# Optimization experiments

Hardware: AMD Instinct MI355X
Metric: run time of the kernel (lower is better)

## Reference

```python
import jax, jax.numpy as jnp
import numpy as np

C = 100000
D = 512
KEEP_RATIO = 0.5
EPS = 1.1920929e-07  # torch.finfo(float32).eps
K = max(1, int(C * KEEP_RATIO))


def _l2norm(x):
    # F.normalize(dim=-1): x / max(||x||, eps)
    n = jnp.linalg.norm(x, axis=-1, keepdims=True)
    return x / jnp.maximum(n, EPS)


def setup_inputs() -> dict:
    key = jax.random.key(0)
    k1, k2, k3 = jax.random.split(key, 3)
    tensor = jax.random.normal(k1, (1024, D), dtype=jnp.float32)
    target = jax.random.randint(k2, (1024,), 0, C, dtype=jnp.int32)
    # xavier_normal_ on (C, D): std = sqrt(2 / (C + D))
    std = np.sqrt(2.0 / (C + D)).astype(np.float32)
    weight = jax.random.normal(k3, (C, D), dtype=jnp.float32) * std
    return {"tensor": tensor, "target": target, "weight": weight}


def reference(tensor, target, weight):
    # --- target mining (no-grad in original) ---
    t_n = _l2norm(tensor)            # (B, D)
    w_n = _l2norm(weight)            # (C, D)
    # max over batch of cosine similarity -> per-class score (C,)
    scores = jnp.max(jnp.einsum("bd,cd->bc", t_n, w_n), axis=0)
    # ground-truth classes always kept
    scores = scores.at[target].set(2.0)
    _, topk_idx = jax.lax.top_k(scores, K)
    subsample = jnp.sort(topk_idx)                       # (K,) ascending
    # remap targets into subsampled index space (targets guaranteed present)
    new_target = jnp.searchsorted(subsample, target).astype(jnp.int32)
    # --- head ---
    w_sub = weight[subsample]                            # (K, D) gather
    logits = jnp.einsum("bd,kd->bk", _l2norm(tensor), _l2norm(w_sub))
    return logits, new_target
```

## Files before the change

### kernel.cpp

```cpp
#include <hip/hip_runtime.h>

#define C_CLS 100000
#define D_DIM 512
#define B_ROWS 1024
#define K_KEEP 50000
#define EPS_F 1.1920929e-07f
#define MB_CT 64
#define BAND 2e-3f
#define DELTA 4e-4f
#define RMAX 32768

typedef short v8s __attribute__((ext_vector_type(8)));
typedef float v4f __attribute__((ext_vector_type(4)));

struct Ctrl { unsigned prefix; unsigned need; };

__device__ __forceinline__ unsigned key_of(float f){
  unsigned u = __float_as_uint(f);
  return (u & 0x80000000u) ? ~u : (u | 0x80000000u);
}
__device__ __forceinline__ float key_inv(unsigned k){
  unsigned u = (k & 0x80000000u) ? (k & 0x7FFFFFFFu) : ~k;
  return __uint_as_float(u);
}
__device__ __forceinline__ unsigned short f2bf_rne(float f){
  unsigned u = __float_as_uint(f);
  unsigned r = (u + 0x7FFFu + ((u >> 16) & 1u)) >> 16;
  return (unsigned short)r;
}
__device__ __forceinline__ float bf2f(unsigned short h){
  return __uint_as_float(((unsigned)h) << 16);
}


__global__ __launch_bounds__(64) void norm_t_kernel(const float* __restrict__ t, float* __restrict__ tn,
                                                    unsigned short* __restrict__ tnph, unsigned short* __restrict__ tnpl,
                                                    const int* __restrict__ tgt, unsigned* __restrict__ keys){
  int row = blockIdx.x, lane = threadIdx.x;
  if (lane == 0) atomicMax(&keys[tgt[row]], key_of(2.0f));
  const float4* p = (const float4*)(t + (size_t)row * D_DIM);
  float4 a = p[lane*2+0], b = p[lane*2+1];
  float s = a.x*a.x + a.y*a.y + a.z*a.z + a.w*a.w
          + b.x*b.x + b.y*b.y + b.z*b.z + b.w*b.w;
  #pragma unroll
  for (int off = 32; off; off >>= 1) s += __shfl_xor(s, off);
  float den = fmaxf(sqrtf(s), EPS_F);
  float o[8] = {a.x/den, a.y/den, a.z/den, a.w/den, b.x/den, b.y/den, b.z/den, b.w/den};
  float4* q = (float4*)(tn + (size_t)row * D_DIM);
  q[lane*2+0] = make_float4(o[0],o[1],o[2],o[3]);
  q[lane*2+1] = make_float4(o[4],o[5],o[6],o[7]);
  v8s hv, lv;
  #pragma unroll
  for (int j = 0; j < 8; ++j){
    unsigned short h = f2bf_rne(o[j]);
    hv[j] = (short)h;
    lv[j] = (short)f2bf_rne(o[j] - bf2f(h));
  }
  size_t di = (size_t)((row & ~15) + (lane >> 2)) * 512 + (lane & 3) * 128 + (row & 15) * 8;
  *(v8s*)(tnph + di) = hv;
  *(v8s*)(tnpl + di) = lv;
}

__device__ __forceinline__ void load_a4(const unsigned short* __restrict__ tp, int b0, int ks, int lane, v8s* dst){
  #pragma unroll
  for (int i = 0; i < 4; ++i){
    int t = b0 + i*16 + (ks >> 5);
    dst[i] = *(const v8s*)(tp + (size_t)t * 512 + lane * 8);
  }
}

__global__ __launch_bounds__(256, 2) void mine_kernel(
    const unsigned short* __restrict__ tnph, const unsigned short* __restrict__ tnpl,
    const float* __restrict__ w, unsigned* __restrict__ keys,
    float* __restrict__ S, float* __restrict__ winv_g){
  __shared__ unsigned short lw[MB_CT * D_DIM];
  __shared__ float wn[MB_CT];
  const int tid = threadIdx.x;
  const int lane = tid & 63;
  const int cb = blockIdx.x * MB_CT;
  #pragma unroll
  for (int st = 0; st < 16; ++st){
    int g = tid + st * 256;
    int row = g >> 6, fc = g & 63;
    int c = cb + row; if (c >= C_CLS) c = C_CLS - 1;
    const float4* src = (const float4*)(w + (size_t)c * D_DIM + fc * 8);
    float4 v0 = src[0], v1 = src[1];
    float vv[8] = {v0.x,v0.y,v0.z,v0.w,v1.x,v1.y,v1.z,v1.w};
    float s = 0.f;
    #pragma unroll
    for (int j = 0; j < 8; ++j) s += vv[j]*vv[j];
    #pragma unroll
    for (int off = 32; off; off >>= 1) s += __shfl_xor(s, off);
    if (lane == 0) wn[row] = 1.0f / fmaxf(sqrtf(s), EPS_F);
    v8s hv;
    #pragma unroll
    for (int j = 0; j < 8; ++j) hv[j] = (short)f2bf_rne(vv[j]);
    int csw = fc ^ (row & 7);
    *(v8s*)&lw[(size_t)row * D_DIM + csw * 8] = hv;
  }
  __syncthreads();
  if (tid < MB_CT && cb + tid < C_CLS) winv_g[cb + tid] = wn[tid];

  const int wv = tid >> 6;
  const int lr = lane & 15, lg = lane >> 4;
  const int bbase = wv * 256;
  float runmax[4] = {-1e30f,-1e30f,-1e30f,-1e30f};
  v4f acc[4][4];
  #pragma unroll
  for (int j = 0; j < 4; ++j)
    #pragma unroll
    for (int i = 0; i < 4; ++i) acc[j][i] = (v4f){0.f,0.f,0.f,0.f};

  v8s cah[4], cal[4];
  load_a4(tnph, bbase, 0, lane, cah);
  load_a4(tnpl, bbase, 0, lane, cal);

  for (int it = 0; it < 64; ++it){
    const int chunk = it >> 4, ks = (it & 15) << 5;
    v8s nah[4], nal[4];
    if (it < 63){
      int nit = it + 1;
      int nb0 = bbase + (nit >> 4) * 64, nks = (nit & 15) << 5;
      load_a4(tnph, nb0, nks, lane, nah);
      load_a4(tnpl, nb0, nks, lane, nal);
    }
    v8s bh[4];
    #pragma unroll
    for (int j = 0; j < 4; ++j){
      int row = j*16 + lr;
      int ch = ((ks >> 3) + lg) ^ (lr & 7);
      bh[j] = *(const v8s*)&lw[(size_t)row * D_DIM + ch * 8];
    }
    #pragma unroll
    for (int j = 0; j < 4; ++j)
      #pragma unroll
      for (int i = 0; i < 4; ++i){
        acc[j][i] = __builtin_amdgcn_mfma_f32_16x16x32_bf16(cah[i], bh[j], acc[j][i], 0, 0, 0);
        acc[j][i] = __builtin_amdgcn_mfma_f32_16x16x32_bf16(cal[i], bh[j], acc[j][i], 0, 0, 0);
      }
    if ((it & 15) == 15){
      int b0 = bbase + chunk * 64;
      #pragma unroll
      for (int j = 0; j < 4; ++j){
        float m = acc[j][0][0];
        #pragma unroll
        for (int i = 0; i < 4; ++i)
          #pragma unroll
          for (int r = 0; r < 4; ++r) m = fmaxf(m, acc[j][i][r]);
        runmax[j] = fmaxf(runmax[j], m);
        int cls = cb + j*16 + lr;
        if (cls < C_CLS){
          #pragma unroll
          for (int i = 0; i < 4; ++i){
            float4 v = make_float4(acc[j][i][0], acc[j][i][1], acc[j][i][2], acc[j][i][3]);
            *(float4*)(S + (size_t)cls * B_ROWS + b0 + i*16 + lg*4) = v;
          }
        }
        #pragma unroll
        for (int i = 0; i < 4; ++i) acc[j][i] = (v4f){0.f,0.f,0.f,0.f};
      }
    }
    if (it < 63){
      #pragma unroll
      for (int i = 0; i < 4; ++i){ cah[i] = nah[i]; cal[i] = nal[i]; }
    }
  }
  #pragma unroll
  for (int j = 0; j < 4; ++j){
    float m = runmax[j];
    m = fmaxf(m, __shfl_xor(m, 16));
    m = fmaxf(m, __shfl_xor(m, 32));
    int cls = cb + j*16 + lr;
    if (lg == 0 && cls < C_CLS)
      atomicMax(&keys[cls], key_of(m * wn[j*16 + lr]));
  }
}

__global__ __launch_bounds__(256) void histsel_kernel(const unsigned* __restrict__ keys, unsigned* __restrict__ hist,
                                                      unsigned* __restrict__ done, Ctrl* __restrict__ ctrl, int shift){
  __shared__ unsigned h[256];
  __shared__ int lastf;
  int t = threadIdx.x;
  h[t] = 0u;
  __syncthreads();
  unsigned himask = (shift >= 24) ? 0u : (0xFFFFFFFFu << (shift + 8));
  unsigned prefix = (shift == 24) ? 0u : (ctrl->prefix & himask);
  for (int c = blockIdx.x * 256 + t; c < C_CLS; c += gridDim.x * 256){
    unsigned k = keys[c];
    if ((k & himask) == prefix) atomicAdd(&h[(k >> shift) & 255], 1u);
  }
  __syncthreads();
  if (h[t]) atomicAdd(&hist[t], h[t]);
  __threadfence();
  if (t == 0) lastf = (atomicAdd(done, 1u) == (unsigned)(gridDim.x - 1));
  __syncthreads();
  if (lastf){
    unsigned v = __hip_atomic_load(&hist[t], __ATOMIC_RELAXED, __HIP_MEMORY_SCOPE_AGENT);
    h[t] = v;
    __syncthreads();
    if (t == 0){
      unsigned need = (shift == 24) ? (unsigned)K_KEEP : ctrl->need;
      unsigned pfx  = (shift == 24) ? 0u : ctrl->prefix;
      unsigned cum = 0; int b;
      for (b = 255; b >= 0; --b){
        if (cum + h[b] >= need) break;
        cum += h[b];
      }
      if (b < 0) b = 0;
      ctrl->prefix = pfx | ((unsigned)b << shift);
      ctrl->need = need - cum;
      __hip_atomic_store(done, 0u, __ATOMIC_RELAXED, __HIP_MEMORY_SCOPE_AGENT);
    }
    __hip_atomic_store(&hist[t], 0u, __ATOMIC_RELAXED, __HIP_MEMORY_SCOPE_AGENT);
  }
}

__global__ void band_kernel(const unsigned* __restrict__ keys, const Ctrl* __restrict__ ctrl,
                            int* __restrict__ rlist, int* __restrict__ rcount){
  int c = blockIdx.x * 256 + threadIdx.x;
  if (c >= C_CLS) return;
  unsigned k = keys[c];
  if (k == key_of(2.0f)) return;
  float t = key_inv(ctrl->prefix);
  if (fabsf(key_inv(k) - t) <= BAND){
    int i = atomicAdd(rcount, 1);
    if (i < RMAX) rlist[i] = c;
  }
}

__global__ __launch_bounds__(256) void refine_kernel(
    const float* __restrict__ tn, const float* __restrict__ w,
    const float* __restrict__ winv, const float* __restrict__ S,
    const int* __restrict__ rlist, const int* __restrict__ rcount,
    unsigned* __restrict__ keys){
  __shared__ float red[256];
  __shared__ double dred[256];
  __shared__ int cand[32];
  __shared__ int ncand;
  int n = *rcount; if (n > RMAX) n = RMAX;
  int t = threadIdx.x;
  for (int i = blockIdx.x; i < n; i += gridDim.x){
    int c = rlist[i];
    const v4f* srow = (const v4f*)(S + (size_t)c * B_ROWS);
    v4f sv = srow[t];
    float m = fmaxf(fmaxf(sv[0],sv[1]), fmaxf(sv[2],sv[3]));
    red[t] = m; __syncthreads();
    for (int off2 = 128; off2; off2 >>= 1){
      if (t < off2) red[t] = fmaxf(red[t], red[t+off2]);
      __syncthreads();
    }
    float thr = red[0] - DELTA;
    if (t == 0) ncand = 0;
    __syncthreads();
    #pragma unroll
    for (int e = 0; e < 4; ++e){
      if (sv[e] >= thr){
        int ci = atomicAdd(&ncand, 1);
        if (ci < 32) cand[ci] = t*4 + e;
      }
    }
    __syncthreads();
    int nc = ncand; if (nc > 32) nc = 32;
    const float* wrow = w + (size_t)c * D_DIM;
    double w0 = (double)wrow[2*t], w1 = (double)wrow[2*t+1];
    double best = -1e300;
    for (int q = 0; q < nc; ++q){
      int b = cand[q];
      const float* tr = tn + (size_t)b * D_DIM;
      double p = fma((double)tr[2*t], w0, (double)tr[2*t+1] * w1);
      dred[t] = p; __syncthreads();
      for (int off2 = 128; off2; off2 >>= 1){
        if (t < off2) dred[t] += dred[t+off2];
        __syncthreads();
      }
      if (t == 0) best = fmax(best, dred[0]);
      __syncthreads();
    }
    if (t == 0) keys[c] = key_of((float)(best * (double)winv[c]));
    __syncthreads();
  }
}

__global__ __launch_bounds__(256) void scanA_kernel(const unsigned* __restrict__ keys, const Ctrl* __restrict__ ctrl,
                                                    uint2* __restrict__ bsum2, unsigned* __restrict__ done2, int nb){
  __shared__ unsigned red[256];
  __shared__ int lastf;
  int t = threadIdx.x;
  unsigned T = ctrl->prefix;
  int base = blockIdx.x * 1024 + t * 4;
  unsigned pack = 0;
  #pragma unroll
  for (int j = 0; j < 4; ++j){
    int c = base + j;
    if (c < C_CLS){
      unsigned k = keys[c];
      if (k > T) pack += 0x10000u;
      else if (k == T) pack += 1u;
    }
  }
  red[t] = pack; __syncthreads();
  for (int off = 128; off; off >>= 1){
    if (t < off) red[t] += red[t + off];
    __syncthreads();
  }
  if (t == 0) bsum2[blockIdx.x] = make_uint2(red[0] >> 16, red[0] & 0xFFFFu);
  __threadfence();
  if (t == 0) lastf = (atomicAdd(done2, 1u) == (unsigned)(gridDim.x - 1));
  __syncthreads();
  if (lastf && t == 0){
    unsigned rg = 0, re = 0;
    for (int i = 0; i < nb; ++i){
      unsigned vx = __hip_atomic_load(&bsum2[i].x, __ATOMIC_RELAXED, __HIP_MEMORY_SCOPE_AGENT);
      unsigned vy = __hip_atomic_load(&bsum2[i].y, __ATOMIC_RELAXED, __HIP_MEMORY_SCOPE_AGENT);
      __hip_atomic_store(&bsum2[i].x, rg, __ATOMIC_RELAXED, __HIP_MEMORY_SCOPE_AGENT);
      __hip_atomic_store(&bsum2[i].y, re, __ATOMIC_RELAXED, __HIP_MEMORY_SCOPE_AGENT);
      rg += vx; re += vy;
    }
    __hip_atomic_store(done2, 0u, __ATOMIC_RELAXED, __HIP_MEMORY_SCOPE_AGENT);
  }
}

__global__ __launch_bounds__(256) void scanC_kernel(const unsigned* __restrict__ keys, const Ctrl* __restrict__ ctrl,
                                                    const uint2* __restrict__ bsum2, unsigned* __restrict__ pos,
                                                    int* __restrict__ sel){
  __shared__ unsigned ls[256];
  int t = threadIdx.x;
  unsigned T = ctrl->prefix, need = ctrl->need;
  int base = blockIdx.x * 1024 + t * 4;
  unsigned gtv[4], eqv[4], pack = 0;
  #pragma unroll
  for (int j = 0; j < 4; ++j){
    int c = base + j;
    unsigned k = (c < C_CLS) ? keys[c] : 0u;
    gtv[j] = (c < C_CLS && k > T) ? 1u : 0u;
    eqv[j] = (c < C_CLS && k == T) ? 1u : 0u;
    pack += (gtv[j] << 16) + eqv[j];
  }
  ls[t] = pack; __syncthreads();
  for (int off = 1; off < 256; off <<= 1){
    unsigned v = (t >= off) ? ls[t - off] : 0u;
    __syncthreads();
    ls[t] += v;
    __syncthreads();
  }
  unsigned excl = ls[t] - pack;
  uint2 bs = bsum2[blockIdx.x];
  unsigned gtx = bs.x + (excl >> 16);
  unsigned eqx = bs.y + (excl & 0xFFFFu);
  #pragma unroll
  for (int j = 0; j < 4; ++j){
    int c = base + j;
    if (c < C_CLS){
      unsigned p = gtx + (eqx < need ? eqx : need);
      pos[c] = p;
      if (gtv[j] || (eqv[j] && eqx < need)) sel[p] = c;
      gtx += gtv[j]; eqx += eqv[j];
    }
  }
}

__global__ void ntgt_kernel(const int* __restrict__ tgt, const unsigned* __restrict__ pos, float* __restrict__ out){
  int b = blockIdx.x * 256 + threadIdx.x;
  if (b < B_ROWS) out[(size_t)B_ROWS * K_KEEP + b] = (float)pos[tgt[b]];
}

__global__ __launch_bounds__(256) void head_copy_kernel(const float* __restrict__ S, const float* __restrict__ winv,
                                                        const int* __restrict__ sel, float* __restrict__ out){
  __shared__ float tile[64][68];
  __shared__ float wsc[64];
  int k0 = blockIdx.x * 64;
  int b0 = blockIdx.y * 64;
  int tid = threadIdx.x;
  int nk = K_KEEP - k0; if (nk > 64) nk = 64;
  if (tid < 64){
    int kk = k0 + tid;
    wsc[tid] = (kk < K_KEEP) ? winv[sel[kk]] : 0.f;
  }
  int i = tid >> 2, part = tid & 3;
  if (i < nk){
    int c = sel[k0 + i];
    const float4* src = (const float4*)(S + (size_t)c * B_ROWS + b0 + part * 16);
    #pragma unroll
    for (int p = 0; p < 4; ++p)
      *(float4*)&tile[i][part*16 + 4*p] = src[p];
  }
  __syncthreads();
  int bb = tid >> 2, q = tid & 3;
  size_t orow = (size_t)(b0 + bb) * K_KEEP + k0;
  #pragma unroll
  for (int t4 = 0; t4 < 4; ++t4){
    int k = q*16 + t4*4;
    if (k + 3 < nk){
      float4 v = make_float4(tile[k+0][bb]*wsc[k+0], tile[k+1][bb]*wsc[k+1],
                             tile[k+2][bb]*wsc[k+2], tile[k+3][bb]*wsc[k+3]);
      *(float4*)(out + orow + k) = v;
    } else {
      for (int e = 0; e < 4; ++e)
        if (k + e < nk) out[orow + k + e] = tile[k+e][bb]*wsc[k+e];
    }
  }
}

extern "C" void kernel_launch(void* const* d_in, const int* in_sizes, int n_in,
                              void* d_out, int out_size, void* d_ws, size_t ws_size,
                              hipStream_t stream){
  const float* tensor = (const float*)d_in[0];
  const int*   target = (const int*)d_in[1];
  const float* weight = (const float*)d_in[2];
  float* out = (float*)d_out;

  char* ws = (char*)d_ws;
  size_t off = 0;
  auto carve = [&](size_t bytes) -> char* {
    char* p = ws + off;
    off = (off + bytes + 511) & ~(size_t)511;
    return p;
  };
  float*          tn   = (float*)carve((size_t)B_ROWS * D_DIM * 4);
  unsigned short* tnph = (unsigned short*)carve((size_t)B_ROWS * D_DIM * 2);
  unsigned short* tnpl = (unsigned short*)carve((size_t)B_ROWS * D_DIM * 2);
  float*          winv = (float*)carve((size_t)C_CLS * 4);
  size_t zs = off;
  unsigned* keys   = (unsigned*)carve((size_t)C_CLS * 4);
  unsigned* hist   = (unsigned*)carve(256 * 4);
  unsigned* done   = (unsigned*)carve(64);
  unsigned* done2  = (unsigned*)carve(64);
  int*      rcount = (int*)carve(64);
  size_t ze = off;
  Ctrl*     ctrl   = (Ctrl*)carve(64);
  uint2*    bsum2  = (uint2*)carve(128 * 8);
  int*      rlist  = (int*)carve((size_t)RMAX * 4);
  unsigned* pos    = (unsigned*)carve((size_t)C_CLS * 4);
  int*      sel    = (int*)carve((size_t)K_KEEP * 4);
  float*    S      = (float*)carve((size_t)C_CLS * B_ROWS * 4);
  (void)in_sizes; (void)n_in; (void)out_size; (void)ws_size;

  hipMemsetAsync(ws + zs, 0, ze - zs, stream);

  norm_t_kernel<<<B_ROWS, 64, 0, stream>>>(tensor, tn, tnph, tnpl, target, keys);

  mine_kernel<<<(C_CLS + MB_CT - 1) / MB_CT, 256, 0, stream>>>(tnph, tnpl, weight, keys, S, winv);

  for (int shift = 24; shift >= 0; shift -= 8)
    histsel_kernel<<<128, 256, 0, stream>>>(keys, hist, done, ctrl, shift);

  band_kernel<<<(C_CLS + 255) / 256, 256, 0, stream>>>(keys, ctrl, rlist, rcount);
  refine_kernel<<<2048, 256, 0, stream>>>(tn, weight, winv, S, rlist, rcount, keys);

  for (int shift = 24; shift >= 0; shift -= 8)
    histsel_kernel<<<128, 256, 0, stream>>>(keys, hist, done, ctrl, shift);

  const int nb = (C_CLS + 1023) / 1024;
  scanA_kernel<<<nb, 256, 0, stream>>>(keys, ctrl, bsum2, done2, nb);
  scanC_kernel<<<nb, 256, 0, stream>>>(keys, ctrl, bsum2, pos, sel);

  ntgt_kernel<<<(B_ROWS + 255) / 256, 256, 0, stream>>>(target, pos, out);
  head_copy_kernel<<<dim3((K_KEEP + 63) / 64, B_ROWS / 64), 256, 0, stream>>>(S, winv, sel, out);
}
```

Before: 669.0 us.

## Double mine class tile to 128 with 512 threads and use nontemporal memory ops

The mining kernel now stages 128 weight classes per block in LDS and runs 8 waves, each covering 128 batch rows against all 128 classes. Each LDS B fragment now feeds fewer MFMAs, but every A fragment loaded from global memory is reused across twice as many classes, which cuts A traffic per class. Weight loads, score-matrix stores, and the head copy's loads and stores become nontemporal to reduce cache pollution on streaming data. The cost is double the LDS per block (128 KB), which may lower occupancy, plus a different register layout.

```diff
diff --git a/kernel.cpp b/kernel.cpp
--- a/kernel.cpp
+++ b/kernel.cpp
@@ -5,7 +5,7 @@
 #define B_ROWS 1024
 #define K_KEEP 50000
 #define EPS_F 1.1920929e-07f
-#define MB_CT 64
+#define MB_CT 128
 #define BAND 2e-3f
 #define DELTA 4e-4f
 #define RMAX 32768
@@ -61,15 +61,15 @@
   *(v8s*)(tnpl + di) = lv;
 }
 
-__device__ __forceinline__ void load_a4(const unsigned short* __restrict__ tp, int b0, int ks, int lane, v8s* dst){
-  #pragma unroll
-  for (int i = 0; i < 4; ++i){
+__device__ __forceinline__ void load_a2(const unsigned short* __restrict__ tp, int b0, int ks, int lane, v8s* dst){
+  #pragma unroll
+  for (int i = 0; i < 2; ++i){
     int t = b0 + i*16 + (ks >> 5);
     dst[i] = *(const v8s*)(tp + (size_t)t * 512 + lane * 8);
   }
 }
 
-__global__ __launch_bounds__(256, 2) void mine_kernel(
+__global__ __launch_bounds__(512, 2) void mine_kernel(
     const unsigned short* __restrict__ tnph, const unsigned short* __restrict__ tnpl,
     const float* __restrict__ w, unsigned* __restrict__ keys,
     float* __restrict__ S, float* __restrict__ winv_g){
@@ -80,12 +80,13 @@
   const int cb = blockIdx.x * MB_CT;
   #pragma unroll
   for (int st = 0; st < 16; ++st){
-    int g = tid + st * 256;
+    int g = tid + st * 512;
     int row = g >> 6, fc = g & 63;
     int c = cb + row; if (c >= C_CLS) c = C_CLS - 1;
-    const float4* src = (const float4*)(w + (size_t)c * D_DIM + fc * 8);
-    float4 v0 = src[0], v1 = src[1];
-    float vv[8] = {v0.x,v0.y,v0.z,v0.w,v1.x,v1.y,v1.z,v1.w};
+    const v4f* src = (const v4f*)(w + (size_t)c * D_DIM + fc * 8);
+    v4f v0 = __builtin_nontemporal_load(src);
+    v4f v1 = __builtin_nontemporal_load(src + 1);
+    float vv[8] = {v0[0],v0[1],v0[2],v0[3],v1[0],v1[1],v1[2],v1[3]};
     float s = 0.f;
     #pragma unroll
     for (int j = 0; j < 8; ++j) s += vv[j]*vv[j];
@@ -103,70 +104,68 @@
 
   const int wv = tid >> 6;
   const int lr = lane & 15, lg = lane >> 4;
-  const int bbase = wv * 256;
-  float runmax[4] = {-1e30f,-1e30f,-1e30f,-1e30f};
-  v4f acc[4][4];
-  #pragma unroll
-  for (int j = 0; j < 4; ++j)
-    #pragma unroll
-    for (int i = 0; i < 4; ++i) acc[j][i] = (v4f){0.f,0.f,0.f,0.f};
-
-  v8s cah[4], cal[4];
-  load_a4(tnph, bbase, 0, lane, cah);
-  load_a4(tnpl, bbase, 0, lane, cal);
+  const int bbase = wv * 128;
+  float runmax[8] = {-1e30f,-1e30f,-1e30f,-1e30f,-1e30f,-1e30f,-1e30f,-1e30f};
+  v4f acc[8][2];
+  #pragma unroll
+  for (int j = 0; j < 8; ++j)
+    #pragma unroll
+    for (int i = 0; i < 2; ++i) acc[j][i] = (v4f){0.f,0.f,0.f,0.f};
+
+  v8s cah[2], cal[2];
+  load_a2(tnph, bbase, 0, lane, cah);
+  load_a2(tnpl, bbase, 0, lane, cal);
 
   for (int it = 0; it < 64; ++it){
     const int chunk = it >> 4, ks = (it & 15) << 5;
-    v8s nah[4], nal[4];
+    const int b0 = bbase + chunk * 32;
+    v8s nah[2], nal[2];
     if (it < 63){
       int nit = it + 1;
-      int nb0 = bbase + (nit >> 4) * 64, nks = (nit & 15) << 5;
-      load_a4(tnph, nb0, nks, lane, nah);
-      load_a4(tnpl, nb0, nks, lane, nal);
-    }
-    v8s bh[4];
-    #pragma unroll
-    for (int j = 0; j < 4; ++j){
+      int nb0 = bbase + (nit >> 4) * 32, nks = (nit & 15) << 5;
+      load_a2(tnph, nb0, nks, lane, nah);
+      load_a2(tnpl, nb0, nks, lane, nal);
+    }
+    v8s bh[8];
+    #pragma unroll
+    for (int j = 0; j < 8; ++j){
       int row = j*16 + lr;
       int ch = ((ks >> 3) + lg) ^ (lr & 7);
       bh[j] = *(const v8s*)&lw[(size_t)row * D_DIM + ch * 8];
     }
     #pragma unroll
-    for (int j = 0; j < 4; ++j)
+    for (int j = 0; j < 8; ++j)
       #pragma unroll
-      for (int i = 0; i < 4; ++i){
+      for (int i = 0; i < 2; ++i){
         acc[j][i] = __builtin_amdgcn_mfma_f32_16x16x32_bf16(cah[i], bh[j], acc[j][i], 0, 0, 0);
         acc[j][i] = __builtin_amdgcn_mfma_f32_16x16x32_bf16(cal[i], bh[j], acc[j][i], 0, 0, 0);
       }
     if ((it & 15) == 15){
-      int b0 = bbase + chunk * 64;
       #pragma unroll
-      for (int j = 0; j < 4; ++j){
+      for (int j = 0; j < 8; ++j){
         float m = acc[j][0][0];
         #pragma unroll
-        for (int i = 0; i < 4; ++i)
+        for (int i = 0; i < 2; ++i)
           #pragma unroll
           for (int r = 0; r < 4; ++r) m = fmaxf(m, acc[j][i][r]);
         runmax[j] = fmaxf(runmax[j], m);
         int cls = cb + j*16 + lr;
         if (cls < C_CLS){
           #pragma unroll
-          for (int i = 0; i < 4; ++i){
-            float4 v = make_float4(acc[j][i][0], acc[j][i][1], acc[j][i][2], acc[j][i][3]);
-            *(float4*)(S + (size_t)cls * B_ROWS + b0 + i*16 + lg*4) = v;
-          }
+          for (int i = 0; i < 2; ++i)
+            __builtin_nontemporal_store(acc[j][i], (v4f*)(S + (size_t)cls * B_ROWS + b0 + i*16 + lg*4));
         }
         #pragma unroll
-        for (int i = 0; i < 4; ++i) acc[j][i] = (v4f){0.f,0.f,0.f,0.f};
+        for (int i = 0; i < 2; ++i) acc[j][i] = (v4f){0.f,0.f,0.f,0.f};
       }
     }
     if (it < 63){
       #pragma unroll
-      for (int i = 0; i < 4; ++i){ cah[i] = nah[i]; cal[i] = nal[i]; }
-    }
-  }
-  #pragma unroll
-  for (int j = 0; j < 4; ++j){
+      for (int i = 0; i < 2; ++i){ cah[i] = nah[i]; cal[i] = nal[i]; }
+    }
+  }
+  #pragma unroll
+  for (int j = 0; j < 8; ++j){
     float m = runmax[j];
     m = fmaxf(m, __shfl_xor(m, 16));
     m = fmaxf(m, __shfl_xor(m, 32));
@@ -379,10 +378,10 @@
   int i = tid >> 2, part = tid & 3;
   if (i < nk){
     int c = sel[k0 + i];
-    const float4* src = (const float4*)(S + (size_t)c * B_ROWS + b0 + part * 16);
+    const v4f* src = (const v4f*)(S + (size_t)c * B_ROWS + b0 + part * 16);
     #pragma unroll
     for (int p = 0; p < 4; ++p)
-      *(float4*)&tile[i][part*16 + 4*p] = src[p];
+      *(v4f*)&tile[i][part*16 + 4*p] = __builtin_nontemporal_load(src + p);
   }
   __syncthreads();
   int bb = tid >> 2, q = tid & 3;
@@ -391,9 +390,9 @@
   for (int t4 = 0; t4 < 4; ++t4){
     int k = q*16 + t4*4;
     if (k + 3 < nk){
-      float4 v = make_float4(tile[k+0][bb]*wsc[k+0], tile[k+1][bb]*wsc[k+1],
-                             tile[k+2][bb]*wsc[k+2], tile[k+3][bb]*wsc[k+3]);
-      *(float4*)(out + orow + k) = v;
+      v4f v = (v4f){tile[k+0][bb]*wsc[k+0], tile[k+1][bb]*wsc[k+1],
+                    tile[k+2][bb]*wsc[k+2], tile[k+3][bb]*wsc[k+3]};
+      __builtin_nontemporal_store(v, (v4f*)(out + orow + k));
     } else {
       for (int e = 0; e < 4; ++e)
         if (k + e < nk) out[orow + k + e] = tile[k+e][bb]*wsc[k+e];
@@ -439,7 +438,7 @@
 
   norm_t_kernel<<<B_ROWS, 64, 0, stream>>>(tensor, tn, tnph, tnpl, target, keys);
 
-  mine_kernel<<<(C_CLS + MB_CT - 1) / MB_CT, 256, 0, stream>>>(tnph, tnpl, weight, keys, S, winv);
+  mine_kernel<<<(C_CLS + MB_CT - 1) / MB_CT, 512, 0, stream>>>(tnph, tnpl, weight, keys, S, winv);
 
   for (int shift = 24; shift >= 0; shift -= 8)
     histsel_kernel<<<128, 256, 0, stream>>>(keys, hist, done, ctrl, shift);
```

After: 935.6 us. 39.8% more time.
